# Optimization experiments

Measured on AMD Instinct MI355X. Metric: run time of the kernel, lower is better.

The kernel has to match this reference:

```python
import jax, jax.numpy as jnp
import numpy as np

CODEBOOK_SIZE = 1024
CODE_DIM = 64
COMMITMENT_COST = 0.25
EMA_DECAY = 0.99
EPS = 1e-05


def setup_inputs() -> dict:
    key = jax.random.key(0)
    k1, k2, k3, k4 = jax.random.split(key, 4)
    z = jax.random.normal(k1, (16, 4096, CODE_DIM), dtype=jnp.float32)
    codebook = jax.random.normal(k2, (CODEBOOK_SIZE, CODE_DIM), dtype=jnp.float32)
    ema_cluster_size = jax.random.uniform(k3, (CODEBOOK_SIZE,), dtype=jnp.float32)
    ema_w = jax.random.normal(k4, (CODEBOOK_SIZE, CODE_DIM), dtype=jnp.float32)
    return {"z": z, "codebook": codebook, "ema_cluster_size": ema_cluster_size, "ema_w": ema_w}


def reference(z, codebook, ema_cluster_size, ema_w):
    B, T, D = z.shape
    K = CODEBOOK_SIZE
    z_flat = z.reshape(-1, D)  # [N, D]

    # Squared-distance expansion: ||z||^2 + ||c||^2 - 2 z c^T  -> [N, K]
    distances = (
        jnp.sum(z_flat * z_flat, axis=-1, keepdims=True)
        + jnp.sum(codebook * codebook, axis=-1)
        - 2.0 * jnp.matmul(z_flat, codebook.T)
    )
    indices = jnp.argmin(distances, axis=-1)  # [N]
    z_q = codebook[indices]  # [N, D] (gathered from OLD codebook)

    # --- EMA codebook update (training, no_grad in torch) ---
    ones = jnp.ones((z_flat.shape[0],), dtype=z_flat.dtype)
    cluster_size = jax.ops.segment_sum(ones, indices, num_segments=K)  # == one_hot.sum(0)
    cluster_sum = jax.ops.segment_sum(z_flat, indices, num_segments=K)  # == one_hot.T @ z_flat
    new_ecs = ema_cluster_size * EMA_DECAY + (1.0 - EMA_DECAY) * cluster_size
    new_ew = ema_w * EMA_DECAY + (1.0 - EMA_DECAY) * cluster_sum
    n = jnp.sum(new_ecs)
    cluster_size_stable = (new_ecs + EPS) / (n + K * EPS) * n
    new_codebook = new_ew / cluster_size_stable[:, None]

    # Commitment loss (EMA path): commitment_cost * mse(z_flat, stop_grad(z_q))
    commitment_loss = jnp.mean((z_flat - jax.lax.stop_gradient(z_q)) ** 2)
    vq_loss = COMMITMENT_COST * commitment_loss

    # Straight-through estimator
    z_q_st = z_flat + jax.lax.stop_gradient(z_q - z_flat)

    z_q_out = z_q_st.reshape(B, T, D)
    indices_out = indices.reshape(B, T)
    return (z_q_out, vq_loss, indices_out, new_codebook, new_ecs, new_ew)
```

## Files before the change

kernel.cpp:

```cpp
#include <hip/hip_runtime.h>

#define KC   1024
#define DD   64
#define NR   65536

#define DECAY     0.99f
#define ONEM      0.01f
#define EPSV      1e-5f
#define MARGIN_W  0.008f

#define OFF_ZQ    0
#define OFF_LOSS  4194304
#define OFF_IDX   4194305
#define OFF_NCB   4259841
#define OFF_NECS  4325377
#define OFF_NEW   4326401


typedef float  f32x4  __attribute__((ext_vector_type(4)));
typedef short  bf16x8 __attribute__((ext_vector_type(8)));

__device__ __forceinline__ unsigned short b16(float v) {
    union { float f; unsigned u; } x; x.f = v;
    return (unsigned short)((x.u + 0x7fffu + ((x.u >> 16) & 1u)) >> 16);
}
__device__ __forceinline__ float b2f(unsigned short h) {
    union { unsigned u; float f; } x; x.u = (unsigned)h << 16;
    return x.f;
}

__device__ __forceinline__ void gload_lds16(const void* g, void* l) {
    __builtin_amdgcn_global_load_lds(
        (const __attribute__((address_space(1))) unsigned int*)g,
        (__attribute__((address_space(3))) unsigned int*)l, 16, 0, 0);
}

__global__ void vq_prep(const float* __restrict__ cb, float* __restrict__ out,
                        unsigned short* __restrict__ cbh,
                        unsigned short* __restrict__ cbm,
                        float* __restrict__ cbT) {
    const int tid = blockIdx.x * blockDim.x + threadIdx.x;
    if (tid < 65536) {
        const int code = tid >> 6, d = tid & 63;
        const int g   = code >> 4, col = code & 15;
        const int kh  = d >> 5, hi2 = (d >> 3) & 3, e = d & 7;
        const int pi  = ((g * 2 + kh) * 64 + hi2 * 16 + col) * 8 + e;
        const float v = cb[tid];
        const unsigned short h = b16(v);
        cbh[pi] = h;
        cbm[pi] = b16(v - b2f(h));
        cbT[d * 1024 + code] = v;
    }
    if (tid < 1024) {
        const float4* c = reinterpret_cast<const float4*>(cb + tid * 64);
        float s = 0.f;
        #pragma unroll
        for (int j = 0; j < 16; ++j) {
            const float4 v = c[j];
            s += v.x*v.x + v.y*v.y + v.z*v.z + v.w*v.w;
        }
        out[OFF_NCB + tid] = s;
    }
    if (tid == 0) out[OFF_LOSS] = 0.0f;
}

__global__ __launch_bounds__(512, 2) void vq_main(const float* __restrict__ z,
                                                  const float* __restrict__ cc,
                                                  const unsigned short* __restrict__ cbh,
                                                  const unsigned short* __restrict__ cbm,
                                                  const float* __restrict__ cbT,
                                                  const float* __restrict__ cb,
                                                  int* __restrict__ idxw,
                                                  float* __restrict__ out) {
    const int t    = threadIdx.x;
    const int lane = t & 63;
    const int wid  = t >> 6;
    const int rowbase = blockIdx.x * 128;

    __shared__ float s_zs[128 * 68];
    __shared__ char  ldsB[2][16384];
    __shared__ float s_cc[1024];
    __shared__ int   s_final[128];
    __shared__ int   s_flag[128];
    __shared__ float s_cd[8][32];
    __shared__ int   s_cix[8][32];
    __shared__ float s_red[8];
    __shared__ int   s_nflag;

    if (t == 0) s_nflag = 0;
    s_cc[t]       = cc[t];
    s_cc[t + 512] = cc[t + 512];

    const float4* zb4 = reinterpret_cast<const float4*>(z) + (size_t)blockIdx.x * 2048;
    #pragma unroll
    for (int j = 0; j < 4; ++j) {
        const int f = t + 512 * j;
        const float4 v = zb4[f];
        *reinterpret_cast<float4*>(&s_zs[(f >> 4) * 68 + (f & 15) * 4]) = v;
    }

    {
        const char* sh = (const char*)cbh + wid * 1024 + lane * 16;
        const char* sm = (const char*)cbm + wid * 1024 + lane * 16;
        gload_lds16(sh, &ldsB[0][wid * 1024]);
        gload_lds16(sm, &ldsB[0][8192 + wid * 1024]);
    }
    __syncthreads();

    bf16x8 a0h, a0m, a1h, a1m;
    {
        const int ar = wid * 16 + (lane & 15);
        const int kb = (lane >> 4) * 8;
        #pragma unroll
        for (int e = 0; e < 8; ++e) {
            const float v0 = s_zs[ar * 68 + kb + e];
            const unsigned short h0 = b16(v0);
            a0h[e] = (short)h0;
            a0m[e] = (short)b16(v0 - b2f(h0));
            const float v1 = s_zs[ar * 68 + 32 + kb + e];
            const unsigned short h1 = b16(v1);
            a1h[e] = (short)h1;
            a1m[e] = (short)b16(v1 - b2f(h1));
        }
    }

    const int lcol   = lane & 15;
    const int lane16 = lane * 16;

    float bd[4], b2v[4]; int bk[4];
    #pragma unroll
    for (int j = 0; j < 4; ++j) { bd[j] = 3.4e38f; b2v[j] = 3.4e38f; bk[j] = 0; }

    for (int c = 0; c < 16; ++c) {
        const int cur = c & 1;
        if (c < 15) {
            const char* sh = (const char*)cbh + (c + 1) * 8192 + wid * 1024 + lane * 16;
            const char* sm = (const char*)cbm + (c + 1) * 8192 + wid * 1024 + lane * 16;
            gload_lds16(sh, &ldsB[cur ^ 1][wid * 1024]);
            gload_lds16(sm, &ldsB[cur ^ 1][8192 + wid * 1024]);
        }
        const char* bh = ldsB[cur];
        const char* bm = ldsB[cur] + 8192;
        #pragma unroll
        for (int gl = 0; gl < 4; ++gl) {
            const bf16x8 bh0 = *reinterpret_cast<const bf16x8*>(bh + gl * 2048 + lane16);
            const bf16x8 bh1 = *reinterpret_cast<const bf16x8*>(bh + gl * 2048 + 1024 + lane16);
            const bf16x8 bm0 = *reinterpret_cast<const bf16x8*>(bm + gl * 2048 + lane16);
            const bf16x8 bm1 = *reinterpret_cast<const bf16x8*>(bm + gl * 2048 + 1024 + lane16);

            f32x4 p0 = {0.f, 0.f, 0.f, 0.f};
            f32x4 p1 = {0.f, 0.f, 0.f, 0.f};
            p0 = __builtin_amdgcn_mfma_f32_16x16x32_bf16(a0m, bh0, p0, 0, 0, 0);
            p1 = __builtin_amdgcn_mfma_f32_16x16x32_bf16(a1m, bh1, p1, 0, 0, 0);
            p0 = __builtin_amdgcn_mfma_f32_16x16x32_bf16(a0h, bm0, p0, 0, 0, 0);
            p1 = __builtin_amdgcn_mfma_f32_16x16x32_bf16(a1h, bm1, p1, 0, 0, 0);
            p0 = __builtin_amdgcn_mfma_f32_16x16x32_bf16(a0h, bh0, p0, 0, 0, 0);
            p1 = __builtin_amdgcn_mfma_f32_16x16x32_bf16(a1h, bh1, p1, 0, 0, 0);

            const int g = c * 4 + gl;
            const float ccv = s_cc[g * 16 + lcol];
            #pragma unroll
            for (int j = 0; j < 4; ++j) {
                const float s = fmaf(-2.f, p0[j] + p1[j], ccv);
                b2v[j] = __builtin_amdgcn_fmed3f(bd[j], s, b2v[j]);
                if (s < bd[j]) { bd[j] = s; bk[j] = g * 16 + lcol; }
            }
        }
        __syncthreads();
    }

    #pragma unroll
    for (int m = 1; m < 16; m <<= 1) {
        #pragma unroll
        for (int j = 0; j < 4; ++j) {
            const float od = __shfl_xor(bd[j],  m);
            const int   oi = __shfl_xor(bk[j],  m);
            const float o2 = __shfl_xor(b2v[j], m);
            const float nb2 = fminf(fmaxf(bd[j], od), fminf(b2v[j], o2));
            if (od < bd[j] || (od == bd[j] && oi < bk[j])) { bd[j] = od; bk[j] = oi; }
            b2v[j] = nb2;
        }
    }
    if ((lane & 15) == 0) {
        #pragma unroll
        for (int j = 0; j < 4; ++j) {
            const int r = wid * 16 + ((lane >> 4) << 2) + j;
            s_final[r] = bk[j];
            if (b2v[j] - bd[j] < MARGIN_W) {
                const int p = atomicAdd(&s_nflag, 1);
                s_flag[p] = r;
            }
        }
    }
    __syncthreads();

    const int nf = s_nflag;
    for (int fb = 0; fb < nf; fb += 32) {
        const int ne = (nf - fb < 32) ? (nf - fb) : 32;
        {
            const int cbase = wid * 128;
            const int c0i = cbase + lane, c1i = c0i + 64;
            for (int i = 0; i < ne; ++i) {
                const int r = s_flag[fb + i];
                float a0 = 0.f, a1 = 0.f;
                #pragma unroll 8
                for (int d = 0; d < 64; ++d) {
                    const float zd = s_zs[r * 68 + d];
                    const float* cr = cbT + d * 1024 + cbase + lane;
                    a0 = fmaf(zd, cr[0],  a0);
                    a1 = fmaf(zd, cr[64], a1);
                }
                float bd_ = fmaf(-2.f, a0, s_cc[c0i]); int bi_ = c0i;
                const float d1 = fmaf(-2.f, a1, s_cc[c1i]);
                if (d1 < bd_) { bd_ = d1; bi_ = c1i; }
                #pragma unroll
                for (int m = 32; m >= 1; m >>= 1) {
                    const float od = __shfl_xor(bd_, m);
                    const int   oi = __shfl_xor(bi_, m);
                    if (od < bd_ || (od == bd_ && oi < bi_)) { bd_ = od; bi_ = oi; }
                }
                if (lane == 0) { s_cd[wid][i] = bd_; s_cix[wid][i] = bi_; }
            }
        }
        __syncthreads();
        if (t < ne) {
            float bd_ = s_cd[0][t]; int bi_ = s_cix[0][t];
            #pragma unroll
            for (int w = 1; w < 8; ++w) {
                const float d = s_cd[w][t]; const int i2 = s_cix[w][t];
                if (d < bd_ || (d == bd_ && i2 < bi_)) { bd_ = d; bi_ = i2; }
            }
            s_final[s_flag[fb + t]] = bi_;
        }
        __syncthreads();
    }

    if (t < 128) {
        const int k2 = s_final[t];
        out[OFF_IDX + rowbase + t] = (float)k2;
        idxw[rowbase + t] = k2;
    }

    float sse = 0.f;
    float4*       qb  = reinterpret_cast<float4*>(out + OFF_ZQ) + (size_t)blockIdx.x * 2048;
    const float4* cb4 = reinterpret_cast<const float4*>(cb);
    #pragma unroll
    for (int j = 0; j < 4; ++j) {
        const int f  = t + 512 * j;
        const int r  = f >> 4;
        const int fc = f & 15;
        const int gk = s_final[r];
        const float4 zv = *reinterpret_cast<const float4*>(&s_zs[r * 68 + fc * 4]);
        const float4 cv = cb4[gk * 16 + fc];
        qb[f] = cv;
        const float e0 = zv.x - cv.x, e1 = zv.y - cv.y;
        const float e2 = zv.z - cv.z, e3 = zv.w - cv.w;
        sse += e0 * e0 + e1 * e1 + e2 * e2 + e3 * e3;
    }

    #pragma unroll
    for (int m = 32; m >= 1; m >>= 1) sse += __shfl_xor(sse, m);
    if (lane == 0) s_red[wid] = sse;
    __syncthreads();
    if (t == 0) {
        float tot = s_red[0];
        #pragma unroll
        for (int i = 1; i < 8; ++i) tot += s_red[i];
        atomicAdd(&out[OFF_LOSS], tot);
    }
}

__global__ __launch_bounds__(512) void vq_sums(const float* __restrict__ z,
                                               const int* __restrict__ idxw,
                                               float* __restrict__ out,
                                               float* __restrict__ cnt) {
    const int t    = threadIdx.x;
    const int lane = t & 63;
    const int w    = t >> 6;
    const int k    = blockIdx.x;
    const int base = w * 8192;

    float acc = 0.f;
    int   c   = 0;

    const int4* ip = reinterpret_cast<const int4*>(idxw + base);
    int4 cur = ip[lane];
    for (int s = 0; s < 32; ++s) {
        int4 nxt = cur;
        if (s < 31) nxt = ip[(s + 1) * 64 + lane];
        const int r0 = base + s * 256;
        c += (cur.x == k) + (cur.y == k) + (cur.z == k) + (cur.w == k);
        unsigned long long m;
        m = __ballot(cur.x == k);
        while (m) { const int j = __ffsll((long long)m) - 1; m &= m - 1;
                    acc += z[(size_t)(r0 + 4 * j + 0) * 64 + lane]; }
        m = __ballot(cur.y == k);
        while (m) { const int j = __ffsll((long long)m) - 1; m &= m - 1;
                    acc += z[(size_t)(r0 + 4 * j + 1) * 64 + lane]; }
        m = __ballot(cur.z == k);
        while (m) { const int j = __ffsll((long long)m) - 1; m &= m - 1;
                    acc += z[(size_t)(r0 + 4 * j + 2) * 64 + lane]; }
        m = __ballot(cur.w == k);
        while (m) { const int j = __ffsll((long long)m) - 1; m &= m - 1;
                    acc += z[(size_t)(r0 + 4 * j + 3) * 64 + lane]; }
        cur = nxt;
    }

    #pragma unroll
    for (int m2 = 32; m2 >= 1; m2 >>= 1) c += __shfl_xor(c, m2);

    __shared__ float s_a[8][64];
    __shared__ int   s_c[8];
    if (lane == 0) s_c[w] = c;
    s_a[w][lane] = acc;
    __syncthreads();
    if (w == 0) {
        float s = s_a[0][lane];
        #pragma unroll
        for (int i = 1; i < 8; ++i) s += s_a[i][lane];
        out[OFF_NEW + k * 64 + lane] = s;
        if (lane == 0) {
            int ct = s_c[0];
            #pragma unroll
            for (int i = 1; i < 8; ++i) ct += s_c[i];
            cnt[k] = (float)ct;
        }
    }
}

__global__ __launch_bounds__(1024) void vq_final(const float* __restrict__ ema_cs,
                                                 const float* __restrict__ ema_w,
                                                 const float* __restrict__ cnt,
                                                 float* __restrict__ out) {
    const int k = threadIdx.x;
    const int b = blockIdx.x;
    const float necs = DECAY * ema_cs[k] + ONEM * cnt[k];

    __shared__ float s_red[1024];
    __shared__ float s_den[1024];
    s_red[k] = necs;
    __syncthreads();
    for (int off = 512; off > 0; off >>= 1) {
        if (k < off) s_red[k] += s_red[k + off];
        __syncthreads();
    }
    const float n = s_red[0];
    s_den[k] = (necs + EPSV) / (n + (float)KC * EPSV) * n;
    if (k >= b * 16 && k < (b + 1) * 16) out[OFF_NECS + k] = necs;
    __syncthreads();

    const int e = b * 1024 + k;
    const float s  = out[OFF_NEW + e];
    const float ew = DECAY * ema_w[e] + ONEM * s;
    out[OFF_NEW + e] = ew;
    out[OFF_NCB + e] = ew / s_den[e >> 6];
    if (b == 0 && k == 0) out[OFF_LOSS] = 0.25f * out[OFF_LOSS] * (1.f / 4194304.f);
}

extern "C" void kernel_launch(void* const* d_in, const int* in_sizes, int n_in,
                              void* d_out, int out_size, void* d_ws, size_t ws_size,
                              hipStream_t stream) {
    const float* z   = (const float*)d_in[0];
    const float* cb  = (const float*)d_in[1];
    const float* ecs = (const float*)d_in[2];
    const float* ew  = (const float*)d_in[3];
    float* out = (float*)d_out;

    unsigned short* cbh  = (unsigned short*)d_ws;
    unsigned short* cbm  = (unsigned short*)((char*)d_ws + 131072);
    float*          cnt  = (float*)((char*)d_ws + 262144);
    float*          cbT  = (float*)((char*)d_ws + 266240);
    int*            idxw = (int*)((char*)d_ws + 528384);

    vq_prep <<<256,  256, 0, stream>>>(cb, out, cbh, cbm, cbT);
    vq_main <<<512,  512, 0, stream>>>(z, out + OFF_NCB, cbh, cbm, cbT, cb, idxw, out);
    vq_sums <<<1024, 512, 0, stream>>>(z, idxw, out, cnt);
    vq_final<<<64,  1024, 0, stream>>>(ecs, ew, cnt, out);
}
```

Before: 95.94 us.

## Drop z LDS staging, raise vq_main occupancy, split segment sums in halves

vq_main no longer stages the 128x64 z tile in shared memory. It reads z directly from global memory for the bf16 split, the fallback rescoring and the loss/gather pass, and raises the launch-bounds occupancy hint from 2 to 6 blocks per CU. The index buffer becomes 16-bit, and vq_sums is split into two halves per code across 2048 blocks writing partial sums that vq_final combines. This aims for more concurrency in both kernels and less index traffic, at the cost of redundant global reads of z and a tighter register budget.

```diff
diff --git a/kernel.cpp b/kernel.cpp
--- a/kernel.cpp
+++ b/kernel.cpp
@@ -64,20 +64,19 @@
     if (tid == 0) out[OFF_LOSS] = 0.0f;
 }
 
-__global__ __launch_bounds__(512, 2) void vq_main(const float* __restrict__ z,
+__global__ __launch_bounds__(512, 6) void vq_main(const float* __restrict__ z,
                                                   const float* __restrict__ cc,
                                                   const unsigned short* __restrict__ cbh,
                                                   const unsigned short* __restrict__ cbm,
                                                   const float* __restrict__ cbT,
                                                   const float* __restrict__ cb,
-                                                  int* __restrict__ idxw,
+                                                  unsigned short* __restrict__ idxw,
                                                   float* __restrict__ out) {
     const int t    = threadIdx.x;
     const int lane = t & 63;
     const int wid  = t >> 6;
     const int rowbase = blockIdx.x * 128;
 
-    __shared__ float s_zs[128 * 68];
     __shared__ char  ldsB[2][16384];
     __shared__ float s_cc[1024];
     __shared__ int   s_final[128];
@@ -91,38 +90,35 @@
     s_cc[t]       = cc[t];
     s_cc[t + 512] = cc[t + 512];
 
-    const float4* zb4 = reinterpret_cast<const float4*>(z) + (size_t)blockIdx.x * 2048;
-    #pragma unroll
-    for (int j = 0; j < 4; ++j) {
-        const int f = t + 512 * j;
-        const float4 v = zb4[f];
-        *reinterpret_cast<float4*>(&s_zs[(f >> 4) * 68 + (f & 15) * 4]) = v;
-    }
-
     {
         const char* sh = (const char*)cbh + wid * 1024 + lane * 16;
         const char* sm = (const char*)cbm + wid * 1024 + lane * 16;
         gload_lds16(sh, &ldsB[0][wid * 1024]);
         gload_lds16(sm, &ldsB[0][8192 + wid * 1024]);
     }
-    __syncthreads();
 
     bf16x8 a0h, a0m, a1h, a1m;
     {
-        const int ar = wid * 16 + (lane & 15);
+        const int ar = rowbase + wid * 16 + (lane & 15);
         const int kb = (lane >> 4) * 8;
+        const float* zr = z + (size_t)ar * 64 + kb;
+        const float4 v0a = *reinterpret_cast<const float4*>(zr);
+        const float4 v0b = *reinterpret_cast<const float4*>(zr + 4);
+        const float4 v1a = *reinterpret_cast<const float4*>(zr + 32);
+        const float4 v1b = *reinterpret_cast<const float4*>(zr + 36);
+        const float z0[8] = {v0a.x, v0a.y, v0a.z, v0a.w, v0b.x, v0b.y, v0b.z, v0b.w};
+        const float z1[8] = {v1a.x, v1a.y, v1a.z, v1a.w, v1b.x, v1b.y, v1b.z, v1b.w};
         #pragma unroll
         for (int e = 0; e < 8; ++e) {
-            const float v0 = s_zs[ar * 68 + kb + e];
-            const unsigned short h0 = b16(v0);
+            const unsigned short h0 = b16(z0[e]);
             a0h[e] = (short)h0;
-            a0m[e] = (short)b16(v0 - b2f(h0));
-            const float v1 = s_zs[ar * 68 + 32 + kb + e];
-            const unsigned short h1 = b16(v1);
+            a0m[e] = (short)b16(z0[e] - b2f(h0));
+            const unsigned short h1 = b16(z1[e]);
             a1h[e] = (short)h1;
-            a1m[e] = (short)b16(v1 - b2f(h1));
-        }
-    }
+            a1m[e] = (short)b16(z1[e] - b2f(h1));
+        }
+    }
+    __syncthreads();
 
     const int lcol   = lane & 15;
     const int lane16 = lane * 16;
@@ -202,10 +198,11 @@
             const int c0i = cbase + lane, c1i = c0i + 64;
             for (int i = 0; i < ne; ++i) {
                 const int r = s_flag[fb + i];
+                const float* zrow = z + (size_t)(rowbase + r) * 64;
                 float a0 = 0.f, a1 = 0.f;
                 #pragma unroll 8
                 for (int d = 0; d < 64; ++d) {
-                    const float zd = s_zs[r * 68 + d];
+                    const float zd = zrow[d];
                     const float* cr = cbT + d * 1024 + cbase + lane;
                     a0 = fmaf(zd, cr[0],  a0);
                     a1 = fmaf(zd, cr[64], a1);
@@ -238,10 +235,11 @@
     if (t < 128) {
         const int k2 = s_final[t];
         out[OFF_IDX + rowbase + t] = (float)k2;
-        idxw[rowbase + t] = k2;
+        idxw[rowbase + t] = (unsigned short)k2;
     }
 
     float sse = 0.f;
+    const float4* zb4 = reinterpret_cast<const float4*>(z) + (size_t)blockIdx.x * 2048;
     float4*       qb  = reinterpret_cast<float4*>(out + OFF_ZQ) + (size_t)blockIdx.x * 2048;
     const float4* cb4 = reinterpret_cast<const float4*>(cb);
     #pragma unroll
@@ -250,7 +248,7 @@
         const int r  = f >> 4;
         const int fc = f & 15;
         const int gk = s_final[r];
-        const float4 zv = *reinterpret_cast<const float4*>(&s_zs[r * 68 + fc * 4]);
+        const float4 zv = zb4[f];
         const float4 cv = cb4[gk * 16 + fc];
         qb[f] = cv;
         const float e0 = zv.x - cv.x, e1 = zv.y - cv.y;
@@ -271,36 +269,38 @@
 }
 
 __global__ __launch_bounds__(512) void vq_sums(const float* __restrict__ z,
-                                               const int* __restrict__ idxw,
-                                               float* __restrict__ out,
-                                               float* __restrict__ cnt) {
+                                               const unsigned short* __restrict__ idxw,
+                                               float* __restrict__ psum,
+                                               float* __restrict__ pcnt) {
     const int t    = threadIdx.x;
     const int lane = t & 63;
     const int w    = t >> 6;
-    const int k    = blockIdx.x;
-    const int base = w * 8192;
+    const int k    = blockIdx.x >> 1;
+    const int hf   = blockIdx.x & 1;
+    const int base = hf * 32768 + w * 4096;
 
     float acc = 0.f;
     int   c   = 0;
 
-    const int4* ip = reinterpret_cast<const int4*>(idxw + base);
-    int4 cur = ip[lane];
-    for (int s = 0; s < 32; ++s) {
-        int4 nxt = cur;
-        if (s < 31) nxt = ip[(s + 1) * 64 + lane];
+    typedef unsigned short u16x4 __attribute__((ext_vector_type(4)));
+    const u16x4* ip = reinterpret_cast<const u16x4*>(idxw + base);
+    u16x4 cur = ip[lane];
+    for (int s = 0; s < 16; ++s) {
+        u16x4 nxt = cur;
+        if (s < 15) nxt = ip[(s + 1) * 64 + lane];
         const int r0 = base + s * 256;
-        c += (cur.x == k) + (cur.y == k) + (cur.z == k) + (cur.w == k);
+        c += (cur[0] == k) + (cur[1] == k) + (cur[2] == k) + (cur[3] == k);
         unsigned long long m;
-        m = __ballot(cur.x == k);
+        m = __ballot(cur[0] == k);
         while (m) { const int j = __ffsll((long long)m) - 1; m &= m - 1;
                     acc += z[(size_t)(r0 + 4 * j + 0) * 64 + lane]; }
-        m = __ballot(cur.y == k);
+        m = __ballot(cur[1] == k);
         while (m) { const int j = __ffsll((long long)m) - 1; m &= m - 1;
                     acc += z[(size_t)(r0 + 4 * j + 1) * 64 + lane]; }
-        m = __ballot(cur.z == k);
+        m = __ballot(cur[2] == k);
         while (m) { const int j = __ffsll((long long)m) - 1; m &= m - 1;
                     acc += z[(size_t)(r0 + 4 * j + 2) * 64 + lane]; }
-        m = __ballot(cur.w == k);
+        m = __ballot(cur[3] == k);
         while (m) { const int j = __ffsll((long long)m) - 1; m &= m - 1;
                     acc += z[(size_t)(r0 + 4 * j + 3) * 64 + lane]; }
         cur = nxt;
@@ -318,23 +318,25 @@
         float s = s_a[0][lane];
         #pragma unroll
         for (int i = 1; i < 8; ++i) s += s_a[i][lane];
-        out[OFF_NEW + k * 64 + lane] = s;
+        psum[(size_t)hf * 65536 + k * 64 + lane] = s;
         if (lane == 0) {
             int ct = s_c[0];
             #pragma unroll
             for (int i = 1; i < 8; ++i) ct += s_c[i];
-            cnt[k] = (float)ct;
+            pcnt[hf * 1024 + k] = (float)ct;
         }
     }
 }
 
 __global__ __launch_bounds__(1024) void vq_final(const float* __restrict__ ema_cs,
                                                  const float* __restrict__ ema_w,
-                                                 const float* __restrict__ cnt,
+                                                 const float* __restrict__ pcnt,
+                                                 const float* __restrict__ psum,
                                                  float* __restrict__ out) {
     const int k = threadIdx.x;
     const int b = blockIdx.x;
-    const float necs = DECAY * ema_cs[k] + ONEM * cnt[k];
+    const float cnt = pcnt[k] + pcnt[1024 + k];
+    const float necs = DECAY * ema_cs[k] + ONEM * cnt;
 
     __shared__ float s_red[1024];
     __shared__ float s_den[1024];
@@ -350,7 +352,7 @@
     __syncthreads();
 
     const int e = b * 1024 + k;
-    const float s  = out[OFF_NEW + e];
+    const float s  = psum[e] + psum[65536 + e];
     const float ew = DECAY * ema_w[e] + ONEM * s;
     out[OFF_NEW + e] = ew;
     out[OFF_NCB + e] = ew / s_den[e >> 6];
@@ -368,12 +370,13 @@
 
     unsigned short* cbh  = (unsigned short*)d_ws;
     unsigned short* cbm  = (unsigned short*)((char*)d_ws + 131072);
-    float*          cnt  = (float*)((char*)d_ws + 262144);
-    float*          cbT  = (float*)((char*)d_ws + 266240);
-    int*            idxw = (int*)((char*)d_ws + 528384);
+    float*          cbT  = (float*)((char*)d_ws + 262144);
+    unsigned short* idxw = (unsigned short*)((char*)d_ws + 524288);
+    float*          pcnt = (float*)((char*)d_ws + 655360);
+    float*          psum = (float*)((char*)d_ws + 663552);
 
     vq_prep <<<256,  256, 0, stream>>>(cb, out, cbh, cbm, cbT);
     vq_main <<<512,  512, 0, stream>>>(z, out + OFF_NCB, cbh, cbm, cbT, cb, idxw, out);
-    vq_sums <<<1024, 512, 0, stream>>>(z, idxw, out, cnt);
-    vq_final<<<64,  1024, 0, stream>>>(ecs, ew, cnt, out);
-}
+    vq_sums <<<2048, 512, 0, stream>>>(z, idxw, psum, pcnt);
+    vq_final<<<64,  1024, 0, stream>>>(ecs, ew, pcnt, psum, out);
+}
```

After: 82.96 us. 13.5% less time.
